# Performance work log

Hardware: AMD Instinct MI355X
Metric: run time of the kernel (lower is better)

## Reference

```python
import jax, jax.numpy as jnp
import numpy as np

N = 100000
E = 3200000
HEADS = 4
DH = 16  # per-head dim
IN = 300
OUT2 = 32
SLOPE = 0.2  # PyG GATConv leaky_relu negative slope


def setup_inputs() -> dict:
    key = jax.random.key(0)
    ks = jax.random.split(key, 10)
    x = jax.random.normal(ks[0], (N, IN), dtype=jnp.float32)
    edge_index = jax.random.randint(ks[1], (2, E), 0, N, dtype=jnp.int64)
    sec_order_edge_index = jax.random.randint(ks[2], (2, E), 0, N, dtype=jnp.int64)
    # GATConv(300, 16, heads=4) params
    W1 = jax.random.normal(ks[3], (IN, HEADS * DH), dtype=jnp.float32) * (1.0 / np.sqrt(IN))
    att_src = jax.random.normal(ks[4], (HEADS, DH), dtype=jnp.float32) * 0.1
    att_dst = jax.random.normal(ks[5], (HEADS, DH), dtype=jnp.float32) * 0.1
    b1 = jnp.zeros((HEADS * DH,), dtype=jnp.float32)
    # GCNConv(64, 32) params
    W2 = jax.random.normal(ks[6], (HEADS * DH, OUT2), dtype=jnp.float32) * (1.0 / np.sqrt(HEADS * DH))
    b2 = jnp.zeros((OUT2,), dtype=jnp.float32)
    return {"x": x, "W1": W1, "att_src": att_src, "att_dst": att_dst, "b1": b1,
            "W2": W2, "b2": b2, "edge_index": edge_index,
            "sec_order_edge_index": sec_order_edge_index}


def _add_self_loops(edge_index, n):
    loop = jnp.arange(n, dtype=edge_index.dtype)
    src = jnp.concatenate([edge_index[0], loop])
    dst = jnp.concatenate([edge_index[1], loop])
    return src, dst


def _gat(x, W1, att_src, att_dst, b1, edge_index):
    n = x.shape[0]
    src, dst = _add_self_loops(edge_index, n)
    h = (x @ W1).reshape(n, HEADS, DH)                    # [N,H,D]
    a_s = jnp.einsum('nhd,hd->nh', h, att_src)            # [N,H]
    a_d = jnp.einsum('nhd,hd->nh', h, att_dst)
    e = jax.nn.leaky_relu(a_s[src] + a_d[dst], SLOPE)     # [Et,H]
    # segment softmax over edges grouped by destination node
    m = jax.ops.segment_max(e, dst, num_segments=n)       # [N,H]
    ex = jnp.exp(e - m[dst])
    denom = jax.ops.segment_sum(ex, dst, num_segments=n)  # [N,H] (>0: self-loops)
    alpha = ex / denom[dst]                               # [Et,H]
    out = jax.ops.segment_sum(h[src] * alpha[:, :, None], dst, num_segments=n)
    return out.reshape(n, HEADS * DH) + b1


def _gcn(x, W2, b2, edge_index):
    n = x.shape[0]
    src, dst = _add_self_loops(edge_index, n)
    deg = jax.ops.segment_sum(jnp.ones_like(dst, dtype=x.dtype), dst, num_segments=n)
    dinv = jnp.where(deg > 0, jax.lax.rsqrt(deg), 0.0)
    norm = dinv[src] * dinv[dst]                          # [Et]
    h = x @ W2                                            # [N,32]
    out = jax.ops.segment_sum(h[src] * norm[:, None], dst, num_segments=n)
    return out + b2


def reference(x, W1, att_src, att_dst, b1, W2, b2, edge_index, sec_order_edge_index):
    x1 = jax.nn.relu(_gat(x, W1, att_src, att_dst, b1, edge_index))
    # F.dropout with training=False is identity (eval mode)
    return _gcn(x1, W2, b2, sec_order_edge_index)
```

## Files before the change

### kernel.cpp

```cpp
#include <hip/hip_runtime.h>
#include <hip/hip_fp16.h>

#define N_NODES 100000
#define N_EDGES 3200000
#define TOT_E   (N_EDGES + N_NODES)
#define HEADS   4
#define DH      16
#define IN_F    300
#define HID     64
#define OUT2    32
#define SLOPE   0.2f
#define NBK     256
#define GSZ     391
#define EBLK    4096
#define NBA     ((TOT_E + EBLK - 1) / EBLK)

typedef _Float16 f16x8 __attribute__((ext_vector_type(8)));
typedef float    f32x4 __attribute__((ext_vector_type(4)));

__global__ void k_wcvt(const float* __restrict__ W1, __half* __restrict__ BT16) {
    int idx = blockIdx.x * 256 + threadIdx.x;
    if (idx >= HID * 320) return;
    int n = idx / 320, k = idx - n * 320;
    BT16[idx] = (k < IN_F) ? __float2half(W1[(size_t)k * HID + n]) : __float2half(0.f);
}

#define G1_BM 128
#define G1_BK 64
#define G1_NS 5

__global__ __launch_bounds__(256) void k_gemm1(const float* __restrict__ x,
                                               const __half* __restrict__ BT16,
                                               __half* __restrict__ h16) {
    __shared__ _Float16 At[G1_BM][G1_BK];
    __shared__ _Float16 Bt[HID][G1_BK];
    const int t = threadIdx.x;
    const int lane = t & 63, w = t >> 6;
    const int lr = lane & 15, lg = lane >> 4;
    const int row0 = blockIdx.x * G1_BM;
    const int wrow = w * 32;

    int arow[4], auc[4];
    const float* axp[4];
#pragma unroll
    for (int m = 0; m < 4; m++) {
        int id = t + m * 256;
        arow[m] = id >> 3; auc[m] = id & 7;
        int gr = row0 + arow[m];
        gr = (gr < N_NODES) ? gr : (N_NODES - 1);
        axp[m] = x + (size_t)gr * IN_F + auc[m] * 8;
    }
    int bn[2], buc[2];
    const __half* bxp[2];
#pragma unroll
    for (int q = 0; q < 2; q++) {
        int id = t + q * 256;
        bn[q] = id >> 3; buc[q] = id & 7;
        bxp[q] = BT16 + bn[q] * (G1_BK * G1_NS) + buc[q] * 8;
    }

    float4 ar[4][2];
    uint4  br[2];

    auto loadS = [&](int kb) {
        if (kb + G1_BK <= IN_F) {
#pragma unroll
            for (int m = 0; m < 4; m++) {
                ar[m][0] = *(const float4*)(axp[m] + kb);
                ar[m][1] = *(const float4*)(axp[m] + kb + 4);
            }
        } else {
#pragma unroll
            for (int m = 0; m < 4; m++) {
                float v[8];
#pragma unroll
                for (int e = 0; e < 8; e++) {
                    int k = kb + auc[m] * 8 + e;
                    v[e] = (k < IN_F) ? axp[m][kb + e] : 0.f;
                }
                ar[m][0] = make_float4(v[0], v[1], v[2], v[3]);
                ar[m][1] = make_float4(v[4], v[5], v[6], v[7]);
            }
        }
#pragma unroll
        for (int q = 0; q < 2; q++) br[q] = *(const uint4*)(bxp[q] + kb);
    };

    auto writeS = [&]() {
#pragma unroll
        for (int m = 0; m < 4; m++) {
            f16x8 pk;
            pk[0] = (_Float16)ar[m][0].x; pk[1] = (_Float16)ar[m][0].y;
            pk[2] = (_Float16)ar[m][0].z; pk[3] = (_Float16)ar[m][0].w;
            pk[4] = (_Float16)ar[m][1].x; pk[5] = (_Float16)ar[m][1].y;
            pk[6] = (_Float16)ar[m][1].z; pk[7] = (_Float16)ar[m][1].w;
            *(f16x8*)&At[arow[m]][(auc[m] ^ (arow[m] & 7)) << 3] = pk;
        }
#pragma unroll
        for (int q = 0; q < 2; q++)
            *(uint4*)&Bt[bn[q]][(buc[q] ^ (bn[q] & 7)) << 3] = br[q];
    };

    f32x4 acc[2][4];
#pragma unroll
    for (int mt = 0; mt < 2; mt++)
#pragma unroll
        for (int nt = 0; nt < 4; nt++) acc[mt][nt] = (f32x4){0.f, 0.f, 0.f, 0.f};

    loadS(0);
    for (int s = 0; s < G1_NS; s++) {
        __syncthreads();
        writeS();
        if (s + 1 < G1_NS) loadS((s + 1) * G1_BK);
        __syncthreads();
#pragma unroll
        for (int ks = 0; ks < 2; ks++) {
            const int u = ks * 4 + lg;
            f16x8 af[2], bf[4];
#pragma unroll
            for (int mt = 0; mt < 2; mt++) {
                int r = wrow + mt * 16 + lr;
                af[mt] = *(const f16x8*)&At[r][(u ^ (r & 7)) << 3];
            }
#pragma unroll
            for (int nt = 0; nt < 4; nt++) {
                int n = nt * 16 + lr;
                bf[nt] = *(const f16x8*)&Bt[n][(u ^ (n & 7)) << 3];
            }
#pragma unroll
            for (int mt = 0; mt < 2; mt++)
#pragma unroll
                for (int nt = 0; nt < 4; nt++)
                    acc[mt][nt] = __builtin_amdgcn_mfma_f32_16x16x32_f16(
                        af[mt], bf[nt], acc[mt][nt], 0, 0, 0);
        }
    }

#pragma unroll
    for (int mt = 0; mt < 2; mt++) {
#pragma unroll
        for (int rg = 0; rg < 4; rg++) {
            int gr = row0 + wrow + mt * 16 + lg * 4 + rg;
            if (gr < N_NODES) {
#pragma unroll
                for (int nt = 0; nt < 4; nt++)
                    h16[(size_t)gr * HID + nt * 16 + lr] =
                        __float2half((float)acc[mt][nt][rg]);
            }
        }
    }
}

__global__ void k_scores(const __half* __restrict__ h16,
                         const float* __restrict__ att_src,
                         const float* __restrict__ att_dst,
                         float* __restrict__ as_ad) {
    int tid = blockIdx.x * blockDim.x + threadIdx.x;
    if (tid >= N_NODES * HEADS) return;
    int n = tid >> 2, hd = tid & 3;
    const __half* hp = &h16[(size_t)n * HID + hd * DH];
    __half2 hv[8];
    *(float4*)&hv[0] = *(const float4*)hp;
    *(float4*)&hv[4] = *(const float4*)(hp + 8);
    float s = 0.f, d = 0.f;
#pragma unroll
    for (int k = 0; k < 8; k++) {
        float2 f = __half22float2(hv[k]);
        s += f.x * att_src[hd * DH + 2 * k] + f.y * att_src[hd * DH + 2 * k + 1];
        d += f.x * att_dst[hd * DH + 2 * k] + f.y * att_dst[hd * DH + 2 * k + 1];
    }
    as_ad[n * 8 + hd] = s;
    as_ad[n * 8 + 4 + hd] = d;
}

__global__ __launch_bounds__(512) void k_chist(const int* __restrict__ ei1,
                                               const int* __restrict__ ei2,
                                               int* __restrict__ ccnt) {
    __shared__ int hist[NBK];
    int b = blockIdx.x; const int* ei; int* cc;
    if (b < NBA) { ei = ei1; cc = ccnt; }
    else         { ei = ei2; cc = ccnt + NBK; b -= NBA; }
    int t = threadIdx.x;
    if (t < NBK) hist[t] = 0;
    __syncthreads();
    int e0 = b * EBLK;
#pragma unroll
    for (int i = 0; i < 8; i++) {
        int e = e0 + i * 512 + t;
        if (e < TOT_E) {
            int dst = (e < N_EDGES) ? ei[N_EDGES + e] : (e - N_EDGES);
            atomicAdd(&hist[(unsigned int)dst / GSZ], 1);
        }
    }
    __syncthreads();
    if (t < NBK) { int v = hist[t]; if (v) atomicAdd(&cc[t], v); }
}

__global__ __launch_bounds__(512) void k_cscan(const int* __restrict__ ccnt,
                                               int* __restrict__ crp,
                                               int* __restrict__ ccur) {
    __shared__ int sc[512];
    int t = threadIdx.x;
    int idx = t & (NBK - 1);
    int own = ccnt[t];
    sc[t] = own;
    __syncthreads();
    for (int off = 1; off < NBK; off <<= 1) {
        int v = (idx >= off) ? sc[t - off] : 0;
        __syncthreads();
        sc[t] += v;
        __syncthreads();
    }
    int ex = sc[t] - own;
    crp[t] = ex; ccur[t] = ex;
}

__global__ __launch_bounds__(512) void k_binA(const int* __restrict__ ei1,
                                              const int* __restrict__ ei2,
                                              int* __restrict__ ccur,
                                              unsigned int* __restrict__ tmp) {
    __shared__ int hist[NBK];
    __shared__ int base[NBK];
    int b = blockIdx.x; const int* ei; int loff;
    if (b < NBA) { ei = ei1; loff = 0; }
    else         { ei = ei2; loff = 1; b -= NBA; }
    int t = threadIdx.x;
    if (t < NBK) hist[t] = 0;
    __syncthreads();
    unsigned int pk[8]; int cb[8], rk[8];
    int e0 = b * EBLK;
#pragma unroll
    for (int i = 0; i < 8; i++) {
        int e = e0 + i * 512 + t;
        cb[i] = -1;
        if (e < TOT_E) {
            int src, dst;
            if (e < N_EDGES) { src = ei[e]; dst = ei[N_EDGES + e]; }
            else             { src = e - N_EDGES; dst = src; }
            unsigned int c   = (unsigned int)dst / GSZ;
            unsigned int dlo = (unsigned int)dst - c * GSZ;
            cb[i] = (int)c;
            pk[i] = (dlo << 17) | (unsigned int)src;
            rk[i] = atomicAdd(&hist[c], 1);
        }
    }
    __syncthreads();
    if (t < NBK) {
        int v = hist[t];
        base[t] = v ? atomicAdd(&ccur[loff * NBK + t], v) : 0;
    }
    __syncthreads();
    unsigned int* tp = tmp + (size_t)loff * TOT_E;
#pragma unroll
    for (int i = 0; i < 8; i++)
        if (cb[i] >= 0) tp[base[cb[i]] + rk[i]] = pk[i];
}

__global__ __launch_bounds__(256) void k_binB(const unsigned int* __restrict__ tmp,
                                              const int* __restrict__ crp,
                                              int* __restrict__ rowptr,
                                              int* __restrict__ srcs,
                                              float* __restrict__ dinv) {
    __shared__ int cnt[GSZ + 1];
    __shared__ int sc[512];
    __shared__ int cur[GSZ + 1];
    int blk = blockIdx.x;
    int l = blk >> 8, b = blk & 255;
    int t = threadIdx.x;
    int nbeg = b * GSZ;
    int ncnt = min(GSZ, N_NODES - nbeg);
    const int* crpl = crp + l * NBK;
    int ebeg = crpl[b];
    int eend = (b < NBK - 1) ? crpl[b + 1] : TOT_E;
    const unsigned int* tp = tmp + (size_t)l * TOT_E;
    for (int i = t; i < GSZ + 1; i += 256) cnt[i] = 0;
    __syncthreads();
    for (int e = ebeg + t; e < eend; e += 256)
        atomicAdd(&cnt[tp[e] >> 17], 1);
    __syncthreads();
    int t2 = t + 256;
    sc[t]  = (t  < ncnt) ? cnt[t]  : 0;
    sc[t2] = (t2 < ncnt) ? cnt[t2] : 0;
    __syncthreads();
    for (int off = 1; off < 512; off <<= 1) {
        int v0 = (t  >= off) ? sc[t  - off] : 0;
        int v1 = (t2 >= off) ? sc[t2 - off] : 0;
        __syncthreads();
        sc[t] += v0; sc[t2] += v1;
        __syncthreads();
    }
    for (int i = t; i < ncnt; i += 256) {
        int c = cnt[i];
        int gpos = ebeg + sc[i] - c;
        rowptr[l * N_NODES + nbeg + i] = gpos;
        cur[i] = gpos;
        if (l == 1) dinv[nbeg + i] = rsqrtf((float)c);
    }
    __syncthreads();
    int* so = srcs + (size_t)l * TOT_E;
    for (int e = ebeg + t; e < eend; e += 256) {
        unsigned int p = tp[e];
        int pos = atomicAdd(&cur[p >> 17], 1);
        so[pos] = (int)(p & 0x1FFFF);
    }
}

__global__ __launch_bounds__(256) void k_gat(const __half* __restrict__ h16,
                                             const float* __restrict__ as_ad,
                                             const int* __restrict__ rowptr,
                                             const int* __restrict__ srcs,
                                             const float* __restrict__ b1,
                                             float* __restrict__ x1) {
    int w = (blockIdx.x * 256 + threadIdx.x) >> 6;
    if (w >= N_NODES) return;
    int lane = threadIdx.x & 63;
    int eidx = lane >> 3;
    int cl = lane & 7;
    int hd = cl >> 1;
    int c0 = cl * 8;
    float ad = as_ad[w * 8 + 4 + hd];
    int beg = rowptr[w];
    int end = (w == N_NODES - 1) ? TOT_E : rowptr[w + 1];
    float l = 0.f;
    float a0 = 0.f, a1 = 0.f, a2 = 0.f, a3 = 0.f;
    float a4 = 0.f, a5 = 0.f, a6 = 0.f, a7 = 0.f;
#pragma unroll 2
    for (int j = beg; j < end; j += 8) {
        int je = j + eidx;
        int s = srcs[min(je, end - 1)];
        float4 raw = *(const float4*)&h16[(size_t)s * HID + c0];
        float e = as_ad[s * 8 + hd] + ad;
        e = fminf(fmaxf(e, SLOPE * e), 60.f);
        float p = (je < end) ? __expf(e) : 0.f;
        l += p;
        const __half2* hv = (const __half2*)&raw;
        float2 f0 = __half22float2(hv[0]);
        float2 f1 = __half22float2(hv[1]);
        float2 f2 = __half22float2(hv[2]);
        float2 f3 = __half22float2(hv[3]);
        a0 += p * f0.x; a1 += p * f0.y; a2 += p * f1.x; a3 += p * f1.y;
        a4 += p * f2.x; a5 += p * f2.y; a6 += p * f3.x; a7 += p * f3.y;
    }
    l  += __shfl_xor(l, 8, 64);  l  += __shfl_xor(l, 16, 64);  l  += __shfl_xor(l, 32, 64);
    a0 += __shfl_xor(a0, 8, 64); a0 += __shfl_xor(a0, 16, 64); a0 += __shfl_xor(a0, 32, 64);
    a1 += __shfl_xor(a1, 8, 64); a1 += __shfl_xor(a1, 16, 64); a1 += __shfl_xor(a1, 32, 64);
    a2 += __shfl_xor(a2, 8, 64); a2 += __shfl_xor(a2, 16, 64); a2 += __shfl_xor(a2, 32, 64);
    a3 += __shfl_xor(a3, 8, 64); a3 += __shfl_xor(a3, 16, 64); a3 += __shfl_xor(a3, 32, 64);
    a4 += __shfl_xor(a4, 8, 64); a4 += __shfl_xor(a4, 16, 64); a4 += __shfl_xor(a4, 32, 64);
    a5 += __shfl_xor(a5, 8, 64); a5 += __shfl_xor(a5, 16, 64); a5 += __shfl_xor(a5, 32, 64);
    a6 += __shfl_xor(a6, 8, 64); a6 += __shfl_xor(a6, 16, 64); a6 += __shfl_xor(a6, 32, 64);
    a7 += __shfl_xor(a7, 8, 64); a7 += __shfl_xor(a7, 16, 64); a7 += __shfl_xor(a7, 32, 64);
    if (eidx == 0) {
        float rl = 1.f / l;
        float4 b0 = *(const float4*)&b1[c0];
        float4 b4 = *(const float4*)&b1[c0 + 4];
        float4 o0 = make_float4(fmaxf(a0 * rl + b0.x, 0.f),
                                fmaxf(a1 * rl + b0.y, 0.f),
                                fmaxf(a2 * rl + b0.z, 0.f),
                                fmaxf(a3 * rl + b0.w, 0.f));
        float4 o4 = make_float4(fmaxf(a4 * rl + b4.x, 0.f),
                                fmaxf(a5 * rl + b4.y, 0.f),
                                fmaxf(a6 * rl + b4.z, 0.f),
                                fmaxf(a7 * rl + b4.w, 0.f));
        *(float4*)&x1[(size_t)w * HID + c0] = o0;
        *(float4*)&x1[(size_t)w * HID + c0 + 4] = o4;
    }
}

__global__ __launch_bounds__(256) void k_gemm2(const float* __restrict__ x1,
                                               const float* __restrict__ W2,
                                               const float* __restrict__ dinv,
                                               __half* __restrict__ h2s) {
    __shared__ float wl[HID * OUT2];
    __shared__ float xl[8][HID];
    int t = threadIdx.x;
    for (int i = t; i < HID * OUT2; i += 256) wl[i] = W2[i];
    int row0 = blockIdx.x * 8;
    for (int i = t; i < 8 * HID; i += 256) {
        int rr = i >> 6, kk = i & 63;
        int gr = row0 + rr;
        xl[rr][kk] = (gr < N_NODES) ? x1[(size_t)gr * HID + kk] : 0.f;
    }
    __syncthreads();
    int r = t >> 5, c = t & 31;
    float acc = 0.f;
#pragma unroll 8
    for (int k = 0; k < HID; k++) acc += xl[r][k] * wl[k * OUT2 + c];
    int gr = row0 + r;
    if (gr < N_NODES) h2s[(size_t)gr * OUT2 + c] = __float2half(acc * dinv[gr]);
}

__global__ __launch_bounds__(256) void k_gcn(const __half* __restrict__ h2s,
                                             const float* __restrict__ dinv,
                                             const int* __restrict__ rowptr,
                                             const int* __restrict__ srcs,
                                             const float* __restrict__ b2,
                                             float* __restrict__ out) {
    int w = (blockIdx.x * 256 + threadIdx.x) >> 6;
    if (w >= N_NODES) return;
    int lane = threadIdx.x & 63;
    int eidx = lane >> 2;
    int cq = lane & 3;
    int c0 = cq * 8;
    int beg = rowptr[w];
    int end = (w == N_NODES - 1) ? TOT_E : rowptr[w + 1];
    float a0 = 0.f, a1 = 0.f, a2 = 0.f, a3 = 0.f;
    float a4 = 0.f, a5 = 0.f, a6 = 0.f, a7 = 0.f;
#pragma unroll 2
    for (int j = beg; j < end; j += 16) {
        int je = j + eidx;
        int s = srcs[min(je, end - 1)];
        uint4 raw = *(const uint4*)&h2s[(size_t)s * OUT2 + c0];
        if (je < end) {
            const __half2* hv = (const __half2*)&raw;
            float2 f0 = __half22float2(hv[0]);
            float2 f1 = __half22float2(hv[1]);
            float2 f2 = __half22float2(hv[2]);
            float2 f3 = __half22float2(hv[3]);
            a0 += f0.x; a1 += f0.y; a2 += f1.x; a3 += f1.y;
            a4 += f2.x; a5 += f2.y; a6 += f3.x; a7 += f3.y;
        }
    }
    a0 += __shfl_xor(a0, 4, 64); a0 += __shfl_xor(a0, 8, 64); a0 += __shfl_xor(a0, 16, 64); a0 += __shfl_xor(a0, 32, 64);
    a1 += __shfl_xor(a1, 4, 64); a1 += __shfl_xor(a1, 8, 64); a1 += __shfl_xor(a1, 16, 64); a1 += __shfl_xor(a1, 32, 64);
    a2 += __shfl_xor(a2, 4, 64); a2 += __shfl_xor(a2, 8, 64); a2 += __shfl_xor(a2, 16, 64); a2 += __shfl_xor(a2, 32, 64);
    a3 += __shfl_xor(a3, 4, 64); a3 += __shfl_xor(a3, 8, 64); a3 += __shfl_xor(a3, 16, 64); a3 += __shfl_xor(a3, 32, 64);
    a4 += __shfl_xor(a4, 4, 64); a4 += __shfl_xor(a4, 8, 64); a4 += __shfl_xor(a4, 16, 64); a4 += __shfl_xor(a4, 32, 64);
    a5 += __shfl_xor(a5, 4, 64); a5 += __shfl_xor(a5, 8, 64); a5 += __shfl_xor(a5, 16, 64); a5 += __shfl_xor(a5, 32, 64);
    a6 += __shfl_xor(a6, 4, 64); a6 += __shfl_xor(a6, 8, 64); a6 += __shfl_xor(a6, 16, 64); a6 += __shfl_xor(a6, 32, 64);
    a7 += __shfl_xor(a7, 4, 64); a7 += __shfl_xor(a7, 8, 64); a7 += __shfl_xor(a7, 16, 64); a7 += __shfl_xor(a7, 32, 64);
    if (eidx == 0) {
        float dv = dinv[w];
        float4 b0 = *(const float4*)&b2[c0];
        float4 b4 = *(const float4*)&b2[c0 + 4];
        float4 o0 = make_float4(a0 * dv + b0.x, a1 * dv + b0.y,
                                a2 * dv + b0.z, a3 * dv + b0.w);
        float4 o4 = make_float4(a4 * dv + b4.x, a5 * dv + b4.y,
                                a6 * dv + b4.z, a7 * dv + b4.w);
        *(float4*)&out[(size_t)w * OUT2 + c0] = o0;
        *(float4*)&out[(size_t)w * OUT2 + c0 + 4] = o4;
    }
}

static inline size_t align_up(size_t v, size_t a) { return (v + a - 1) & ~(a - 1); }

extern "C" void kernel_launch(void* const* d_in, const int* in_sizes, int n_in,
                              void* d_out, int out_size, void* d_ws, size_t ws_size,
                              hipStream_t stream) {
    const float* x       = (const float*)d_in[0];
    const float* W1      = (const float*)d_in[1];
    const float* att_src = (const float*)d_in[2];
    const float* att_dst = (const float*)d_in[3];
    const float* b1      = (const float*)d_in[4];
    const float* W2      = (const float*)d_in[5];
    const float* b2      = (const float*)d_in[6];
    const int*   ei1     = (const int*)d_in[7];
    const int*   ei2     = (const int*)d_in[8];
    float* out = (float*)d_out;

    char* p = (char*)d_ws;
    size_t off = 0;
    auto carve = [&](size_t bytes) { void* q = p + off; off = align_up(off + bytes, 256); return q; };
    __half* h16   = (__half*)carve((size_t)N_NODES * HID * 2);
    float* x1     = (float*)carve((size_t)N_NODES * HID * 4);
    __half* h2s   = (__half*)carve((size_t)N_NODES * OUT2 * 2);
    float* as_ad  = (float*)carve((size_t)N_NODES * 8 * 4);
    float* dinv   = (float*)carve((size_t)N_NODES * 4);
    int* rowptr   = (int*)carve((size_t)2 * N_NODES * 4);
    int* srcs     = (int*)carve((size_t)2 * TOT_E * 4);
    int* ccnt     = (int*)carve((size_t)2 * NBK * 4);
    int* crp      = (int*)carve((size_t)2 * NBK * 4);
    int* ccur     = (int*)carve((size_t)2 * NBK * 4);
    __half* BT16  = (__half*)carve((size_t)HID * 320 * 2);
    unsigned int* tmp = (unsigned int*)x1;
    (void)ws_size; (void)in_sizes; (void)n_in; (void)out_size;

    hipMemsetAsync(ccnt, 0, (size_t)2 * NBK * 4, stream);

    k_wcvt<<<(HID * 320 + 255) / 256, 256, 0, stream>>>(W1, BT16);
    k_gemm1<<<(N_NODES + G1_BM - 1) / G1_BM, 256, 0, stream>>>(x, BT16, h16);
    k_scores<<<(N_NODES * HEADS + 255) / 256, 256, 0, stream>>>(h16, att_src, att_dst, as_ad);

    k_chist<<<2 * NBA, 512, 0, stream>>>(ei1, ei2, ccnt);
    k_cscan<<<1, 512, 0, stream>>>(ccnt, crp, ccur);
    k_binA<<<2 * NBA, 512, 0, stream>>>(ei1, ei2, ccur, tmp);
    k_binB<<<2 * NBK, 256, 0, stream>>>(tmp, crp, rowptr, srcs, dinv);

    k_gat<<<N_NODES / 4, 256, 0, stream>>>(h16, as_ad, rowptr, srcs, b1, x1);

    k_gemm2<<<N_NODES / 8, 256, 0, stream>>>(x1, W2, dinv, h2s);

    k_gcn<<<N_NODES / 4, 256, 0, stream>>>(h2s, dinv, rowptr + N_NODES, srcs + TOT_E, b2, out);
}
```

Baseline: 553.9 us.

## Use head-major feature layout and run GAT aggregation per head

Stores the GAT hidden features and attention scores head-major, as [head][node][16], and launches the GAT aggregation as one pass per head, with 16 lanes handling each destination node. Each pass gathers from a 3.2 MB slice rather than the full 12.8 MB table, so more of the random source gathers should hit in cache. In exchange, the edge list and rowptr are read four times and each gather moves only 32 bytes per node. It also adds nontemporal loads for the streamed srcs arrays and nontemporal stores for x1.

```diff
diff --git a/kernel.cpp b/kernel.cpp
--- a/kernel.cpp
+++ b/kernel.cpp
@@ -31,7 +31,7 @@
 
 __global__ __launch_bounds__(256) void k_gemm1(const float* __restrict__ x,
                                                const __half* __restrict__ BT16,
-                                               __half* __restrict__ h16) {
+                                               __half* __restrict__ hH) {
     __shared__ _Float16 At[G1_BM][G1_BK];
     __shared__ _Float16 Bt[HID][G1_BK];
     const int t = threadIdx.x;
@@ -144,21 +144,21 @@
             if (gr < N_NODES) {
 #pragma unroll
                 for (int nt = 0; nt < 4; nt++)
-                    h16[(size_t)gr * HID + nt * 16 + lr] =
+                    hH[((size_t)nt * N_NODES + gr) * DH + lr] =
                         __float2half((float)acc[mt][nt][rg]);
             }
         }
     }
 }
 
-__global__ void k_scores(const __half* __restrict__ h16,
+__global__ void k_scores(const __half* __restrict__ hH,
                          const float* __restrict__ att_src,
                          const float* __restrict__ att_dst,
-                         float* __restrict__ as_ad) {
+                         float* __restrict__ asH, float* __restrict__ adH) {
     int tid = blockIdx.x * blockDim.x + threadIdx.x;
     if (tid >= N_NODES * HEADS) return;
-    int n = tid >> 2, hd = tid & 3;
-    const __half* hp = &h16[(size_t)n * HID + hd * DH];
+    int hd = tid / N_NODES;
+    const __half* hp = &hH[(size_t)tid * DH];
     __half2 hv[8];
     *(float4*)&hv[0] = *(const float4*)hp;
     *(float4*)&hv[4] = *(const float4*)(hp + 8);
@@ -169,8 +169,8 @@
         s += f.x * att_src[hd * DH + 2 * k] + f.y * att_src[hd * DH + 2 * k + 1];
         d += f.x * att_dst[hd * DH + 2 * k] + f.y * att_dst[hd * DH + 2 * k + 1];
     }
-    as_ad[n * 8 + hd] = s;
-    as_ad[n * 8 + 4 + hd] = d;
+    asH[tid] = s;
+    adH[tid] = d;
 }
 
 __global__ __launch_bounds__(512) void k_chist(const int* __restrict__ ei1,
@@ -305,20 +305,25 @@
     }
 }
 
-__global__ __launch_bounds__(256) void k_gat(const __half* __restrict__ h16,
-                                             const float* __restrict__ as_ad,
+#define GAT_BPH (N_NODES / 16)
+
+__global__ __launch_bounds__(256) void k_gat(const __half* __restrict__ hH,
+                                             const float* __restrict__ asH,
+                                             const float* __restrict__ adH,
                                              const int* __restrict__ rowptr,
                                              const int* __restrict__ srcs,
                                              const float* __restrict__ b1,
                                              float* __restrict__ x1) {
-    int w = (blockIdx.x * 256 + threadIdx.x) >> 6;
-    if (w >= N_NODES) return;
-    int lane = threadIdx.x & 63;
-    int eidx = lane >> 3;
-    int cl = lane & 7;
-    int hd = cl >> 1;
-    int c0 = cl * 8;
-    float ad = as_ad[w * 8 + 4 + hd];
+    int bid = blockIdx.x;
+    int hd = bid / GAT_BPH;
+    int blk = bid - hd * GAT_BPH;
+    int w = blk * 16 + (threadIdx.x >> 4);
+    int lane = threadIdx.x & 15;
+    int eidx = lane >> 1;
+    int c0 = (lane & 1) * 8;
+    const __half* hT = hH + (size_t)hd * N_NODES * DH;
+    const float* asT = asH + (size_t)hd * N_NODES;
+    float ad = adH[(size_t)hd * N_NODES + w];
     int beg = rowptr[w];
     int end = (w == N_NODES - 1) ? TOT_E : rowptr[w + 1];
     float l = 0.f;
@@ -327,9 +332,9 @@
 #pragma unroll 2
     for (int j = beg; j < end; j += 8) {
         int je = j + eidx;
-        int s = srcs[min(je, end - 1)];
-        float4 raw = *(const float4*)&h16[(size_t)s * HID + c0];
-        float e = as_ad[s * 8 + hd] + ad;
+        int s = __builtin_nontemporal_load(&srcs[min(je, end - 1)]);
+        uint4 raw = *(const uint4*)&hT[(size_t)s * DH + c0];
+        float e = asT[s] + ad;
         e = fminf(fmaxf(e, SLOPE * e), 60.f);
         float p = (je < end) ? __expf(e) : 0.f;
         l += p;
@@ -341,29 +346,30 @@
         a0 += p * f0.x; a1 += p * f0.y; a2 += p * f1.x; a3 += p * f1.y;
         a4 += p * f2.x; a5 += p * f2.y; a6 += p * f3.x; a7 += p * f3.y;
     }
-    l  += __shfl_xor(l, 8, 64);  l  += __shfl_xor(l, 16, 64);  l  += __shfl_xor(l, 32, 64);
-    a0 += __shfl_xor(a0, 8, 64); a0 += __shfl_xor(a0, 16, 64); a0 += __shfl_xor(a0, 32, 64);
-    a1 += __shfl_xor(a1, 8, 64); a1 += __shfl_xor(a1, 16, 64); a1 += __shfl_xor(a1, 32, 64);
-    a2 += __shfl_xor(a2, 8, 64); a2 += __shfl_xor(a2, 16, 64); a2 += __shfl_xor(a2, 32, 64);
-    a3 += __shfl_xor(a3, 8, 64); a3 += __shfl_xor(a3, 16, 64); a3 += __shfl_xor(a3, 32, 64);
-    a4 += __shfl_xor(a4, 8, 64); a4 += __shfl_xor(a4, 16, 64); a4 += __shfl_xor(a4, 32, 64);
-    a5 += __shfl_xor(a5, 8, 64); a5 += __shfl_xor(a5, 16, 64); a5 += __shfl_xor(a5, 32, 64);
-    a6 += __shfl_xor(a6, 8, 64); a6 += __shfl_xor(a6, 16, 64); a6 += __shfl_xor(a6, 32, 64);
-    a7 += __shfl_xor(a7, 8, 64); a7 += __shfl_xor(a7, 16, 64); a7 += __shfl_xor(a7, 32, 64);
-    if (eidx == 0) {
+    l  += __shfl_xor(l, 2, 64);  l  += __shfl_xor(l, 4, 64);  l  += __shfl_xor(l, 8, 64);
+    a0 += __shfl_xor(a0, 2, 64); a0 += __shfl_xor(a0, 4, 64); a0 += __shfl_xor(a0, 8, 64);
+    a1 += __shfl_xor(a1, 2, 64); a1 += __shfl_xor(a1, 4, 64); a1 += __shfl_xor(a1, 8, 64);
+    a2 += __shfl_xor(a2, 2, 64); a2 += __shfl_xor(a2, 4, 64); a2 += __shfl_xor(a2, 8, 64);
+    a3 += __shfl_xor(a3, 2, 64); a3 += __shfl_xor(a3, 4, 64); a3 += __shfl_xor(a3, 8, 64);
+    a4 += __shfl_xor(a4, 2, 64); a4 += __shfl_xor(a4, 4, 64); a4 += __shfl_xor(a4, 8, 64);
+    a5 += __shfl_xor(a5, 2, 64); a5 += __shfl_xor(a5, 4, 64); a5 += __shfl_xor(a5, 8, 64);
+    a6 += __shfl_xor(a6, 2, 64); a6 += __shfl_xor(a6, 4, 64); a6 += __shfl_xor(a6, 8, 64);
+    a7 += __shfl_xor(a7, 2, 64); a7 += __shfl_xor(a7, 4, 64); a7 += __shfl_xor(a7, 8, 64);
+    if (lane < 2) {
         float rl = 1.f / l;
-        float4 b0 = *(const float4*)&b1[c0];
-        float4 b4 = *(const float4*)&b1[c0 + 4];
-        float4 o0 = make_float4(fmaxf(a0 * rl + b0.x, 0.f),
-                                fmaxf(a1 * rl + b0.y, 0.f),
-                                fmaxf(a2 * rl + b0.z, 0.f),
-                                fmaxf(a3 * rl + b0.w, 0.f));
-        float4 o4 = make_float4(fmaxf(a4 * rl + b4.x, 0.f),
-                                fmaxf(a5 * rl + b4.y, 0.f),
-                                fmaxf(a6 * rl + b4.z, 0.f),
-                                fmaxf(a7 * rl + b4.w, 0.f));
-        *(float4*)&x1[(size_t)w * HID + c0] = o0;
-        *(float4*)&x1[(size_t)w * HID + c0 + 4] = o4;
+        int cb = hd * DH + c0;
+        float4 b0v = *(const float4*)&b1[cb];
+        float4 b4v = *(const float4*)&b1[cb + 4];
+        f32x4 o0 = {fmaxf(a0 * rl + b0v.x, 0.f),
+                    fmaxf(a1 * rl + b0v.y, 0.f),
+                    fmaxf(a2 * rl + b0v.z, 0.f),
+                    fmaxf(a3 * rl + b0v.w, 0.f)};
+        f32x4 o4 = {fmaxf(a4 * rl + b4v.x, 0.f),
+                    fmaxf(a5 * rl + b4v.y, 0.f),
+                    fmaxf(a6 * rl + b4v.z, 0.f),
+                    fmaxf(a7 * rl + b4v.w, 0.f)};
+        __builtin_nontemporal_store(o0, (f32x4*)&x1[(size_t)w * HID + cb]);
+        __builtin_nontemporal_store(o4, (f32x4*)&x1[(size_t)w * HID + cb + 4]);
     }
 }
 
@@ -409,7 +415,7 @@
 #pragma unroll 2
     for (int j = beg; j < end; j += 16) {
         int je = j + eidx;
-        int s = srcs[min(je, end - 1)];
+        int s = __builtin_nontemporal_load(&srcs[min(je, end - 1)]);
         uint4 raw = *(const uint4*)&h2s[(size_t)s * OUT2 + c0];
         if (je < end) {
             const __half2* hv = (const __half2*)&raw;
@@ -461,10 +467,11 @@
     char* p = (char*)d_ws;
     size_t off = 0;
     auto carve = [&](size_t bytes) { void* q = p + off; off = align_up(off + bytes, 256); return q; };
-    __half* h16   = (__half*)carve((size_t)N_NODES * HID * 2);
+    __half* hH    = (__half*)carve((size_t)HEADS * N_NODES * DH * 2);
     float* x1     = (float*)carve((size_t)N_NODES * HID * 4);
     __half* h2s   = (__half*)carve((size_t)N_NODES * OUT2 * 2);
-    float* as_ad  = (float*)carve((size_t)N_NODES * 8 * 4);
+    float* asH    = (float*)carve((size_t)HEADS * N_NODES * 4);
+    float* adH    = (float*)carve((size_t)HEADS * N_NODES * 4);
     float* dinv   = (float*)carve((size_t)N_NODES * 4);
     int* rowptr   = (int*)carve((size_t)2 * N_NODES * 4);
     int* srcs     = (int*)carve((size_t)2 * TOT_E * 4);
@@ -478,15 +485,15 @@
     hipMemsetAsync(ccnt, 0, (size_t)2 * NBK * 4, stream);
 
     k_wcvt<<<(HID * 320 + 255) / 256, 256, 0, stream>>>(W1, BT16);
-    k_gemm1<<<(N_NODES + G1_BM - 1) / G1_BM, 256, 0, stream>>>(x, BT16, h16);
-    k_scores<<<(N_NODES * HEADS + 255) / 256, 256, 0, stream>>>(h16, att_src, att_dst, as_ad);
+    k_gemm1<<<(N_NODES + G1_BM - 1) / G1_BM, 256, 0, stream>>>(x, BT16, hH);
+    k_scores<<<(N_NODES * HEADS + 255) / 256, 256, 0, stream>>>(hH, att_src, att_dst, asH, adH);
 
     k_chist<<<2 * NBA, 512, 0, stream>>>(ei1, ei2, ccnt);
     k_cscan<<<1, 512, 0, stream>>>(ccnt, crp, ccur);
     k_binA<<<2 * NBA, 512, 0, stream>>>(ei1, ei2, ccur, tmp);
     k_binB<<<2 * NBK, 256, 0, stream>>>(tmp, crp, rowptr, srcs, dinv);
 
-    k_gat<<<N_NODES / 4, 256, 0, stream>>>(h16, as_ad, rowptr, srcs, b1, x1);
+    k_gat<<<HEADS * GAT_BPH, 256, 0, stream>>>(hH, asH, adH, rowptr, srcs, b1, x1);
 
     k_gemm2<<<N_NODES / 8, 256, 0, stream>>>(x1, W2, dinv, h2s);
 
```

Measured after the change: 645.4 us. +16.5%, slower.
